# Kernel optimization log

Hardware: AMD Instinct MI355X
Metric: run time of the kernel (lower is better)

Reference implementation:

```python
import jax, jax.numpy as jnp
import numpy as np

M = 28            # mask head resolution (mask_logit[i] is MxM)
NUM_CLASSES = 80  # max value of cls_idx (mask_image channel count)


def setup_inputs() -> dict:
    key = jax.random.key(0)
    k1, k2, k3, k4, k5, k6, k7 = jax.random.split(key, 7)
    N, H, W = 100, 800, 800
    cx = jax.random.uniform(k1, (N,), minval=0.0, maxval=float(W - 1))
    cy = jax.random.uniform(k2, (N,), minval=0.0, maxval=float(H - 1))
    bw = jax.random.uniform(k3, (N,), minval=20.0, maxval=300.0)
    bh = jax.random.uniform(k4, (N,), minval=20.0, maxval=300.0)
    mask_rois = jnp.stack([cx - bw / 2, cy - bh / 2, cx + bw / 2, cy + bh / 2], axis=1).astype(jnp.float32)
    cls_prob = jax.random.uniform(k5, (N,), dtype=jnp.float32)
    mask_prob = jax.random.normal(k6, (N, M, M), dtype=jnp.float32)
    cls_idx = jax.random.randint(k7, (N,), 1, NUM_CLASSES + 1, dtype=jnp.int32)
    return {"mask_rois": mask_rois, "cls_prob": cls_prob, "mask_prob": mask_prob,
            "cls_idx": cls_idx, "im_h": H, "im_w": W}


def _paste(logit, box, H, W):
    """Bilinear-paste an MxM logit into the full HxW image (== cv2.resize to (w,h)
    then placing at the box, evaluated directly on image pixel coords)."""
    x0, y0, x1, y1 = box[0], box[1], box[2], box[3]  # int32
    w = jnp.maximum(x1 - x0 + 1, 1).astype(jnp.float32)
    h = jnp.maximum(y1 - y0 + 1, 1).astype(jnp.float32)
    xs = jnp.arange(W, dtype=jnp.float32)
    ys = jnp.arange(H, dtype=jnp.float32)
    # cv2 bilinear mapping: src = (dst + 0.5) * (M / size) - 0.5, clamped at borders
    sx = jnp.clip((xs - x0.astype(jnp.float32) + 0.5) * (M / w) - 0.5, 0.0, M - 1.0)
    sy = jnp.clip((ys - y0.astype(jnp.float32) + 0.5) * (M / h) - 0.5, 0.0, M - 1.0)
    ix0 = jnp.floor(sx).astype(jnp.int32); ix1 = jnp.minimum(ix0 + 1, M - 1); fx = sx - ix0
    iy0 = jnp.floor(sy).astype(jnp.int32); iy1 = jnp.minimum(iy0 + 1, M - 1); fy = sy - iy0
    v00 = logit[iy0[:, None], ix0[None, :]]
    v01 = logit[iy0[:, None], ix1[None, :]]
    v10 = logit[iy1[:, None], ix0[None, :]]
    v11 = logit[iy1[:, None], ix1[None, :]]
    val = ((1 - fy)[:, None] * ((1 - fx)[None, :] * v00 + fx[None, :] * v01)
           + fy[:, None] * ((1 - fx)[None, :] * v10 + fx[None, :] * v11))
    xi = jnp.arange(W, dtype=jnp.int32)
    yi = jnp.arange(H, dtype=jnp.int32)
    inside_x = (xi >= jnp.maximum(x0, 0)) & (xi < jnp.minimum(x1 + 1, W))
    inside_y = (yi >= jnp.maximum(y0, 0)) & (yi < jnp.minimum(y1 + 1, H))
    inside = inside_y[:, None] & inside_x[None, :]
    return jnp.where(inside, val, 0.0), inside


def _forward(mask_rois, cls_prob, mask_prob, cls_idx, H, W, thr):
    N = mask_prob.shape[0]
    order = jnp.argsort(-cls_prob)                       # sort by score, descending
    boxes = mask_rois[order].astype(jnp.int32)
    logits = mask_prob[order]
    cls = cls_idx[order].astype(jnp.int32) - 1           # 0-based class ids
    pasted, inside = jax.vmap(lambda l, b: _paste(l, b, H, W))(logits, boxes)  # [N,H,W]

    def step(mask_image, xs):
        logit, ins, c = xs
        mask = (logit > 0) & ins                          # thresholded, in-image crop mask
        prev = mask_image[c]
        msum = jnp.sum(mask).astype(jnp.float32)
        ovl = jnp.sum(mask & prev).astype(jnp.float32)    # overlap with accumulated class mask
        keep = (msum > 0) & (ovl <= thr * msum)           # skip if ratio > threshold
        mask_image = mask_image.at[c].set(prev | (mask & keep))
        return mask_image, keep

    mask_image0 = jnp.zeros((NUM_CLASSES, H, W), dtype=bool)
    _, keep = jax.lax.scan(step, mask_image0, (pasted, inside, cls))

    # compact kept masks to the front (frame_id order); dropped boxes go to slot N (discarded)
    pos = jnp.where(keep, jnp.cumsum(keep.astype(jnp.int32)) - 1, N)
    energy = jnp.where(inside & keep[:, None, None], pasted, 0.0)
    full = jnp.zeros((N + 1, H, W), pasted.dtype).at[pos].set(energy)
    mask_energy = full[:N][None]                          # [1, N, H, W], kept masks first
    keep_inds = jnp.full((N + 1,), -1, jnp.int32).at[pos].set(
        jnp.where(keep, order.astype(jnp.int32), -1))[:N]
    return keep_inds, mask_energy


def reference(mask_rois, cls_prob, mask_prob, cls_idx, im_h, im_w):
    return _forward(mask_rois, cls_prob, mask_prob, cls_idx, int(im_h), int(im_w), 0.3)
```

## Files before the change

kernel.cpp:

```cpp
#include <hip/hip_runtime.h>

#define NINST 100
#define MLOG 28
#define IMG 800
#define LOGSZ (MLOG * MLOG)

#define OFF_ORDER 0
#define OFF_CLS   100
#define OFF_BOX   200
#define OFF_MSUM  600
#define OFF_SLOT  800
#define OFF_NK    900
#define OFF_OVL   1024
#define OFF_MASK  11264
#define ROWW      12
#define MSTRIDE   (ROWW * 304)
#define F4TOT     (NINST * IMG * IMG / 4)
#define NZB       4096

__device__ __forceinline__ bool box_ovl(const int* sb, int a, int b2) {
    int axs = max(sb[4 * a], 0), axe = min(sb[4 * a + 2] + 1, IMG);
    int ays = max(sb[4 * a + 1], 0), aye = min(sb[4 * a + 3] + 1, IMG);
    int bxs = max(sb[4 * b2], 0), bxe = min(sb[4 * b2 + 2] + 1, IMG);
    int bys = max(sb[4 * b2 + 1], 0), bye = min(sb[4 * b2 + 3] + 1, IMG);
    return axs < bxe && bxs < axe && ays < bye && bys < aye;
}

__global__ __launch_bounds__(256) void k_mask(const float* __restrict__ mask_prob,
                                              const float* __restrict__ cls_prob,
                                              const float* __restrict__ rois,
                                              const int* __restrict__ cls_idx,
                                              int* __restrict__ ws) {
    int b = blockIdx.x, tid = threadIdx.x;
    __shared__ float s_p[NINST];
    __shared__ int s_order[NINST];
    __shared__ float lg[LOGSZ];
    __shared__ int red[256];
    if (tid < NINST) s_p[tid] = cls_prob[tid];
    __syncthreads();
    if (tid < NINST) {
        float p = s_p[tid];
        int r = 0;
        for (int j = 0; j < NINST; j++) {
            float q = s_p[j];
            r += (q > p) || (q == p && j < tid);
        }
        s_order[r] = tid;
    }
    __syncthreads();
    int n = b;
    int orig = s_order[n];
    int x0 = (int)rois[4 * orig], y0 = (int)rois[4 * orig + 1];
    int x1 = (int)rois[4 * orig + 2], y1 = (int)rois[4 * orig + 3];
    if (b == 0 && tid < NINST) {
        int o = s_order[tid];
        ws[OFF_ORDER + tid] = o;
        ws[OFF_CLS + tid] = cls_idx[o] - 1;
#pragma unroll
        for (int k = 0; k < 4; k++)
            ws[OFF_BOX + 4 * tid + k] = (int)rois[4 * o + k];
    }
    for (int i = tid; i < LOGSZ; i += 256) lg[i] = mask_prob[orig * LOGSZ + i];
    __syncthreads();
    int xs = max(x0, 0), xe = min(x1 + 1, IMG);
    int ys = max(y0, 0), ye = min(y1 + 1, IMG);
    int wx0 = xs >> 5, nw = ((xe + 31) >> 5) - wx0, nrows = ye - ys;
    float wf = fmaxf((float)(x1 - x0 + 1), 1.f), hf = fmaxf((float)(y1 - y0 + 1), 1.f);
    float rx = 28.f / wf, ry = 28.f / hf;
    unsigned* mb = (unsigned*)(ws + OFF_MASK) + n * MSTRIDE;
    int total = nrows * nw, cnt = 0;
    for (int t = tid; t < total; t += 256) {
        int row = t / nw, wc = t - row * nw;
        int y = ys + row;
        float sy = ((float)y - (float)y0 + 0.5f) * ry - 0.5f;
        sy = fminf(fmaxf(sy, 0.f), 27.f);
        int iy0 = (int)sy, iy1 = min(iy0 + 1, 27);
        float fy = sy - (float)iy0;
        const float* r0 = lg + iy0 * MLOG;
        const float* r1 = lg + iy1 * MLOG;
        unsigned bits = 0u;
        int xbase = (wx0 + wc) << 5;
        int j0 = max(xs - xbase, 0), j1 = min(xe - xbase, 32);
        for (int j = j0; j < j1; j++) {
            int xx = xbase + j;
            float sx = ((float)xx - (float)x0 + 0.5f) * rx - 0.5f;
            sx = fminf(fmaxf(sx, 0.f), 27.f);
            int ix0 = (int)sx, ix1 = min(ix0 + 1, 27);
            float fx = sx - (float)ix0;
            float val = (1.f - fy) * ((1.f - fx) * r0[ix0] + fx * r0[ix1]) +
                        fy * ((1.f - fx) * r1[ix0] + fx * r1[ix1]);
            bits |= (val > 0.f) ? (1u << j) : 0u;
        }
        mb[row * ROWW + wc] = bits;
        cnt += __popc(bits);
    }
    red[tid] = cnt;
    __syncthreads();
    for (int s = 128; s; s >>= 1) {
        if (tid < s) red[tid] += red[tid + s];
        __syncthreads();
    }
    if (tid == 0) ws[OFF_MSUM + n] = red[0];
}

__global__ __launch_bounds__(64) void k_pairs(int* __restrict__ ws) {
    int i = blockIdx.x, j = blockIdx.y, tid = threadIdx.x;
    if (i >= j) return;
    if (ws[OFF_CLS + i] != ws[OFF_CLS + j]) return;
    if (ws[OFF_MSUM + i] == 0 || ws[OFF_MSUM + j] == 0) return;
    const int* bi = ws + OFF_BOX + 4 * i;
    const int* bj = ws + OFF_BOX + 4 * j;
    int ixs = max(bi[0], 0), ixe = min(bi[2] + 1, IMG);
    int iys = max(bi[1], 0), iye = min(bi[3] + 1, IMG);
    int jxs = max(bj[0], 0), jxe = min(bj[2] + 1, IMG);
    int jys = max(bj[1], 0), jye = min(bj[3] + 1, IMG);
    if (!(ixs < jxe && jxs < ixe && iys < jye && jys < iye)) return;
    int iwx0 = ixs >> 5, jwx0 = jxs >> 5;
    int wlo = max(iwx0, jwx0);
    int whi = min((ixe + 31) >> 5, (jxe + 31) >> 5);
    int rlo = max(iys, jys), rhi = min(iye, jye);
    int nw = whi - wlo, nrows = rhi - rlo;
    const unsigned* mi = (const unsigned*)(ws + OFF_MASK) + i * MSTRIDE;
    const unsigned* mj = (const unsigned*)(ws + OFF_MASK) + j * MSTRIDE;
    int total = nrows * nw, cnt = 0;
    for (int t = tid; t < total; t += 64) {
        int row = t / nw, wc = t - row * nw;
        int y = rlo + row, w = wlo + wc;
        cnt += __popc(mi[(y - iys) * ROWW + (w - iwx0)] &
                      mj[(y - jys) * ROWW + (w - jwx0)]);
    }
    for (int off = 32; off; off >>= 1) cnt += __shfl_down(cnt, off);
    if (tid == 0) ws[OFF_OVL + i * NINST + j] = cnt;
}

__global__ __launch_bounds__(256) void k_scan_zero(int* __restrict__ ws, float* __restrict__ out) {
    int b = blockIdx.x, tid = threadIdx.x;
    if (b > 0) {
        float4* outv = (float4*)(out + NINST);
        for (size_t pi = (size_t)(b - 1) * 256 + tid; pi < F4TOT; pi += (size_t)NZB * 256)
            outv[pi] = make_float4(0.f, 0.f, 0.f, 0.f);
        return;
    }
    __shared__ int s_ovl[NINST * NINST];
    __shared__ int s_cls[NINST], s_msum[NINST], s_box[4 * NINST];
    for (int i = tid; i < NINST * NINST; i += 256) s_ovl[i] = ws[OFF_OVL + i];
    for (int i = tid; i < NINST; i += 256) {
        s_cls[i] = ws[OFF_CLS + i];
        s_msum[i] = ws[OFF_MSUM + i];
    }
    for (int i = tid; i < 4 * NINST; i += 256) s_box[i] = ws[OFF_BOX + i];
    __syncthreads();
    if (tid >= 64) return;
    int ln = tid;
    const unsigned* maskbase = (const unsigned*)(ws + OFF_MASK);

    unsigned long long k0 = 0ull, k1 = 0ull;
    for (int n = 0; n < NINST; n++) {
        int msum = s_msum[n];
        if (msum == 0) continue;
        int pb = 64 + ln;
        bool ca = (ln < n) && s_cls[ln] == s_cls[n] && ((k0 >> ln) & 1ull) && box_ovl(s_box, ln, n);
        bool cb = (pb < n) && s_cls[pb] == s_cls[n] && ((k1 >> ln) & 1ull) && box_ovl(s_box, pb, n);
        int oa = ca ? s_ovl[ln * NINST + n] : 0;
        int ob = cb ? s_ovl[pb * NINST + n] : 0;
        int sum = oa + ob, mx = max(oa, ob);
        for (int off = 32; off; off >>= 1) {
            sum += __shfl_down(sum, off);
            mx = max(mx, __shfl_down(mx, off));
        }
        int keep = 0, need = 0;
        if (ln == 0) {
            float t = 0.3f * (float)msum;
            if ((float)sum <= t) keep = 1;
            else if ((float)mx > t) keep = 0;
            else need = 1;
        }
        keep = __shfl(keep, 0);
        need = __shfl(need, 0);
        if (need) {
            unsigned long long ba = __ballot(ca), bb = __ballot(cb);
            int nxs = max(s_box[4 * n], 0), nxe = min(s_box[4 * n + 2] + 1, IMG);
            int nys = max(s_box[4 * n + 1], 0), nye = min(s_box[4 * n + 3] + 1, IMG);
            int wx0 = nxs >> 5, nw = ((nxe + 31) >> 5) - wx0, nrows = nye - nys;
            const unsigned* mn = maskbase + n * MSTRIDE;
            int total = nrows * nw, ovl = 0;
            for (int t2 = ln; t2 < total; t2 += 64) {
                int row = t2 / nw, wc = t2 - row * nw;
                unsigned bits = mn[row * ROWW + wc];
                if (!bits) continue;
                int y = nys + row, wa = wx0 + wc;
                unsigned img = 0;
                unsigned long long rem = ba;
                while (rem) {
                    int m = __ffsll((long long)rem) - 1; rem &= rem - 1;
                    int mys = max(s_box[4 * m + 1], 0), mye = min(s_box[4 * m + 3] + 1, IMG);
                    int mxs = max(s_box[4 * m], 0), mxe = min(s_box[4 * m + 2] + 1, IMG);
                    int mwx0 = mxs >> 5, mnw = ((mxe + 31) >> 5) - mwx0;
                    int rr = y - mys, cc = wa - mwx0;
                    if (rr >= 0 && rr < (mye - mys) && cc >= 0 && cc < mnw)
                        img |= maskbase[m * MSTRIDE + rr * ROWW + cc];
                }
                rem = bb;
                while (rem) {
                    int m0 = __ffsll((long long)rem) - 1; rem &= rem - 1;
                    int m = 64 + m0;
                    int mys = max(s_box[4 * m + 1], 0), mye = min(s_box[4 * m + 3] + 1, IMG);
                    int mxs = max(s_box[4 * m], 0), mxe = min(s_box[4 * m + 2] + 1, IMG);
                    int mwx0 = mxs >> 5, mnw = ((mxe + 31) >> 5) - mwx0;
                    int rr = y - mys, cc = wa - mwx0;
                    if (rr >= 0 && rr < (mye - mys) && cc >= 0 && cc < mnw)
                        img |= maskbase[m * MSTRIDE + rr * ROWW + cc];
                }
                ovl += __popc(bits & img);
            }
            for (int off = 32; off; off >>= 1) ovl += __shfl_down(ovl, off);
            if (ln == 0) keep = ((float)ovl <= 0.3f * (float)msum);
            keep = __shfl(keep, 0);
        }
        if (keep) {
            if (n < 64) k0 |= 1ull << n;
            else k1 |= 1ull << (n - 64);
        }
    }

    int nk = __popcll(k0) + __popcll(k1);
    if (ln == 0) ws[OFF_NK] = nk;
    unsigned long long lm = (ln == 0) ? 0ull : (~0ull >> (64 - ln));
    if ((k0 >> ln) & 1ull) {
        int pos = __popcll(k0 & lm);
        ws[OFF_SLOT + pos] = ln;
        out[pos] = (float)ws[OFF_ORDER + ln];
    }
    if (ln < 36 && ((k1 >> ln) & 1ull)) {
        int pos = __popcll(k0) + __popcll(k1 & lm);
        ws[OFF_SLOT + pos] = 64 + ln;
        out[pos] = (float)ws[OFF_ORDER + 64 + ln];
    }
    for (int s = ln; s < NINST; s += 64)
        if (s >= nk) out[s] = -1.f;
}

__global__ __launch_bounds__(256) void k_box(const float* __restrict__ mask_prob,
                                             const int* __restrict__ ws,
                                             float* __restrict__ out) {
    int slot = blockIdx.y, tid = threadIdx.x;
    if (slot >= ws[OFF_NK]) return;
    int n = ws[OFF_SLOT + slot];
    const int* box = ws + OFF_BOX + 4 * n;
    int x0 = box[0], y0 = box[1], x1 = box[2], y1 = box[3];
    int xs = max(x0, 0), xe = min(x1 + 1, IMG);
    int ys = max(y0, 0), ye = min(y1 + 1, IMG);
    int xa = xs & ~3;
    int w4 = (xe - xa + 3) >> 2;
    int rows = ye - ys;
    int total4 = rows * w4;
    __shared__ float lg[LOGSZ];
    int orig = ws[OFF_ORDER + n];
    for (int i = tid; i < LOGSZ; i += 256) lg[i] = mask_prob[orig * LOGSZ + i];
    __syncthreads();
    float wf = fmaxf((float)(x1 - x0 + 1), 1.f), hf = fmaxf((float)(y1 - y0 + 1), 1.f);
    float rx = 28.f / wf, ry = 28.f / hf;
    float* base = out + NINST + (size_t)slot * (IMG * IMG);
    for (int t = blockIdx.x * 256 + tid; t < total4; t += gridDim.x * 256) {
        int row = t / w4, c4 = t - row * w4;
        int y = ys + row, xb = xa + (c4 << 2);
        float sy = ((float)y - (float)y0 + 0.5f) * ry - 0.5f;
        sy = fminf(fmaxf(sy, 0.f), 27.f);
        int iy0 = (int)sy, iy1 = min(iy0 + 1, 27);
        float fy = sy - (float)iy0;
        const float* r0 = lg + iy0 * MLOG;
        const float* r1 = lg + iy1 * MLOG;
        float v[4];
#pragma unroll
        for (int j = 0; j < 4; j++) {
            int xx = xb + j;
            float val = 0.f;
            if (xx >= xs && xx < xe) {
                float sx = ((float)xx - (float)x0 + 0.5f) * rx - 0.5f;
                sx = fminf(fmaxf(sx, 0.f), 27.f);
                int ix0 = (int)sx, ix1 = min(ix0 + 1, 27);
                float fx = sx - (float)ix0;
                val = (1.f - fy) * ((1.f - fx) * r0[ix0] + fx * r0[ix1]) +
                      fy * ((1.f - fx) * r1[ix0] + fx * r1[ix1]);
            }
            v[j] = val;
        }
        *(float4*)(base + (size_t)y * IMG + xb) = make_float4(v[0], v[1], v[2], v[3]);
    }
}

extern "C" void kernel_launch(void* const* d_in, const int* in_sizes, int n_in,
                              void* d_out, int out_size, void* d_ws, size_t ws_size,
                              hipStream_t stream) {
    const float* rois      = (const float*)d_in[0];
    const float* cls_prob  = (const float*)d_in[1];
    const float* mask_prob = (const float*)d_in[2];
    const int*   cls_idx   = (const int*)d_in[3];
    int* ws = (int*)d_ws;
    float* out = (float*)d_out;

    k_mask<<<dim3(NINST), dim3(256), 0, stream>>>(mask_prob, cls_prob, rois, cls_idx, ws);
    k_pairs<<<dim3(NINST, NINST), dim3(64), 0, stream>>>(ws);
    k_scan_zero<<<dim3(NZB + 1), dim3(256), 0, stream>>>(ws, out);
    k_box<<<dim3(91, NINST), dim3(256), 0, stream>>>(mask_prob, ws, out);
}
```

Baseline: 357.1 us.

## Fuse pair-overlap, keep scan and paste into one persistent kernel with grid barriers

Replaces the pairs, scan-plus-zero and box kernels with a single persistent kernel of 512 blocks that uses software grid barriers. Pair overlaps are compacted into a small atomic list rather than a dense 100x100 matrix. Each output plane is written exactly once, as either zeros or pasted values, which removes the separate full-image zeroing pass and its double write. The risks are spin-barrier deadlock if all 512 blocks are not co-resident, and a fallback to the slow path when the pair list overflows its 256 capacity.

After: 470.2 us. 31.7% more time.

```diff
diff --git a/kernel.cpp b/kernel.cpp
--- a/kernel.cpp
+++ b/kernel.cpp
@@ -4,6 +4,10 @@
 #define MLOG 28
 #define IMG 800
 #define LOGSZ (MLOG * MLOG)
+#define NBLK2 512
+#define PCAP  256
+#define PL4   (IMG * IMG / 4)
+#define CH4   (PL4 / 5)
 
 #define OFF_ORDER 0
 #define OFF_CLS   100
@@ -11,12 +15,14 @@
 #define OFF_MSUM  600
 #define OFF_SLOT  800
 #define OFF_NK    900
-#define OFF_OVL   1024
+#define OFF_NPAIR 901
+#define OFF_BAR   904
+#define OFF_PAIRS 1024
 #define OFF_MASK  11264
 #define ROWW      12
 #define MSTRIDE   (ROWW * 304)
-#define F4TOT     (NINST * IMG * IMG / 4)
-#define NZB       4096
+
+#define AGENT __HIP_MEMORY_SCOPE_AGENT
 
 __device__ __forceinline__ bool box_ovl(const int* sb, int a, int b2) {
     int axs = max(sb[4 * a], 0), axe = min(sb[4 * a + 2] + 1, IMG);
@@ -24,6 +30,17 @@
     int bxs = max(sb[4 * b2], 0), bxe = min(sb[4 * b2 + 2] + 1, IMG);
     int bys = max(sb[4 * b2 + 1], 0), bye = min(sb[4 * b2 + 3] + 1, IMG);
     return axs < bxe && bxs < axe && ays < bye && bys < aye;
+}
+
+__device__ __forceinline__ void gbar(int* cnt, int nblk) {
+    __syncthreads();
+    if (threadIdx.x == 0) {
+        __threadfence();
+        __hip_atomic_fetch_add(cnt, 1, __ATOMIC_RELEASE, AGENT);
+        while (__hip_atomic_load(cnt, __ATOMIC_ACQUIRE, AGENT) < nblk)
+            __builtin_amdgcn_s_sleep(8);
+    }
+    __syncthreads();
 }
 
 __global__ __launch_bounds__(256) void k_mask(const float* __restrict__ mask_prob,
@@ -52,13 +69,20 @@
     int orig = s_order[n];
     int x0 = (int)rois[4 * orig], y0 = (int)rois[4 * orig + 1];
     int x1 = (int)rois[4 * orig + 2], y1 = (int)rois[4 * orig + 3];
-    if (b == 0 && tid < NINST) {
-        int o = s_order[tid];
-        ws[OFF_ORDER + tid] = o;
-        ws[OFF_CLS + tid] = cls_idx[o] - 1;
+    if (b == 0) {
+        if (tid == 0) {
+            ws[OFF_NPAIR] = 0;
+            ws[OFF_BAR] = 0;
+            ws[OFF_BAR + 1] = 0;
+        }
+        if (tid < NINST) {
+            int o = s_order[tid];
+            ws[OFF_ORDER + tid] = o;
+            ws[OFF_CLS + tid] = cls_idx[o] - 1;
 #pragma unroll
-        for (int k = 0; k < 4; k++)
-            ws[OFF_BOX + 4 * tid + k] = (int)rois[4 * o + k];
+            for (int k = 0; k < 4; k++)
+                ws[OFF_BOX + 4 * tid + k] = (int)rois[4 * o + k];
+        }
     }
     for (int i = tid; i < LOGSZ; i += 256) lg[i] = mask_prob[orig * LOGSZ + i];
     __syncthreads();
@@ -103,189 +127,216 @@
     if (tid == 0) ws[OFF_MSUM + n] = red[0];
 }
 
-__global__ __launch_bounds__(64) void k_pairs(int* __restrict__ ws) {
-    int i = blockIdx.x, j = blockIdx.y, tid = threadIdx.x;
-    if (i >= j) return;
-    if (ws[OFF_CLS + i] != ws[OFF_CLS + j]) return;
-    if (ws[OFF_MSUM + i] == 0 || ws[OFF_MSUM + j] == 0) return;
-    const int* bi = ws + OFF_BOX + 4 * i;
-    const int* bj = ws + OFF_BOX + 4 * j;
-    int ixs = max(bi[0], 0), ixe = min(bi[2] + 1, IMG);
-    int iys = max(bi[1], 0), iye = min(bi[3] + 1, IMG);
-    int jxs = max(bj[0], 0), jxe = min(bj[2] + 1, IMG);
-    int jys = max(bj[1], 0), jye = min(bj[3] + 1, IMG);
-    if (!(ixs < jxe && jxs < ixe && iys < jye && jys < iye)) return;
-    int iwx0 = ixs >> 5, jwx0 = jxs >> 5;
-    int wlo = max(iwx0, jwx0);
-    int whi = min((ixe + 31) >> 5, (jxe + 31) >> 5);
-    int rlo = max(iys, jys), rhi = min(iye, jye);
-    int nw = whi - wlo, nrows = rhi - rlo;
-    const unsigned* mi = (const unsigned*)(ws + OFF_MASK) + i * MSTRIDE;
-    const unsigned* mj = (const unsigned*)(ws + OFF_MASK) + j * MSTRIDE;
-    int total = nrows * nw, cnt = 0;
-    for (int t = tid; t < total; t += 64) {
-        int row = t / nw, wc = t - row * nw;
-        int y = rlo + row, w = wlo + wc;
-        cnt += __popc(mi[(y - iys) * ROWW + (w - iwx0)] &
-                      mj[(y - jys) * ROWW + (w - jwx0)]);
-    }
-    for (int off = 32; off; off >>= 1) cnt += __shfl_down(cnt, off);
-    if (tid == 0) ws[OFF_OVL + i * NINST + j] = cnt;
-}
-
-__global__ __launch_bounds__(256) void k_scan_zero(int* __restrict__ ws, float* __restrict__ out) {
+__global__ __launch_bounds__(256, 2) void k_fused(const float* __restrict__ mask_prob,
+                                                  int* __restrict__ ws,
+                                                  float* __restrict__ out) {
     int b = blockIdx.x, tid = threadIdx.x;
-    if (b > 0) {
-        float4* outv = (float4*)(out + NINST);
-        for (size_t pi = (size_t)(b - 1) * 256 + tid; pi < F4TOT; pi += (size_t)NZB * 256)
-            outv[pi] = make_float4(0.f, 0.f, 0.f, 0.f);
-        return;
-    }
     __shared__ int s_ovl[NINST * NINST];
     __shared__ int s_cls[NINST], s_msum[NINST], s_box[4 * NINST];
-    for (int i = tid; i < NINST * NINST; i += 256) s_ovl[i] = ws[OFF_OVL + i];
-    for (int i = tid; i < NINST; i += 256) {
-        s_cls[i] = ws[OFF_CLS + i];
-        s_msum[i] = ws[OFF_MSUM + i];
-    }
-    for (int i = tid; i < 4 * NINST; i += 256) s_box[i] = ws[OFF_BOX + i];
-    __syncthreads();
-    if (tid >= 64) return;
-    int ln = tid;
+    __shared__ float lg[LOGSZ];
     const unsigned* maskbase = (const unsigned*)(ws + OFF_MASK);
 
-    unsigned long long k0 = 0ull, k1 = 0ull;
-    for (int n = 0; n < NINST; n++) {
-        int msum = s_msum[n];
-        if (msum == 0) continue;
-        int pb = 64 + ln;
-        bool ca = (ln < n) && s_cls[ln] == s_cls[n] && ((k0 >> ln) & 1ull) && box_ovl(s_box, ln, n);
-        bool cb = (pb < n) && s_cls[pb] == s_cls[n] && ((k1 >> ln) & 1ull) && box_ovl(s_box, pb, n);
-        int oa = ca ? s_ovl[ln * NINST + n] : 0;
-        int ob = cb ? s_ovl[pb * NINST + n] : 0;
-        int sum = oa + ob, mx = max(oa, ob);
-        for (int off = 32; off; off >>= 1) {
-            sum += __shfl_down(sum, off);
-            mx = max(mx, __shfl_down(mx, off));
-        }
-        int keep = 0, need = 0;
-        if (ln == 0) {
-            float t = 0.3f * (float)msum;
-            if ((float)sum <= t) keep = 1;
-            else if ((float)mx > t) keep = 0;
-            else need = 1;
-        }
-        keep = __shfl(keep, 0);
-        need = __shfl(need, 0);
-        if (need) {
-            unsigned long long ba = __ballot(ca), bb = __ballot(cb);
-            int nxs = max(s_box[4 * n], 0), nxe = min(s_box[4 * n + 2] + 1, IMG);
-            int nys = max(s_box[4 * n + 1], 0), nye = min(s_box[4 * n + 3] + 1, IMG);
-            int wx0 = nxs >> 5, nw = ((nxe + 31) >> 5) - wx0, nrows = nye - nys;
-            const unsigned* mn = maskbase + n * MSTRIDE;
-            int total = nrows * nw, ovl = 0;
-            for (int t2 = ln; t2 < total; t2 += 64) {
-                int row = t2 / nw, wc = t2 - row * nw;
-                unsigned bits = mn[row * ROWW + wc];
-                if (!bits) continue;
-                int y = nys + row, wa = wx0 + wc;
-                unsigned img = 0;
-                unsigned long long rem = ba;
-                while (rem) {
-                    int m = __ffsll((long long)rem) - 1; rem &= rem - 1;
-                    int mys = max(s_box[4 * m + 1], 0), mye = min(s_box[4 * m + 3] + 1, IMG);
-                    int mxs = max(s_box[4 * m], 0), mxe = min(s_box[4 * m + 2] + 1, IMG);
-                    int mwx0 = mxs >> 5, mnw = ((mxe + 31) >> 5) - mwx0;
-                    int rr = y - mys, cc = wa - mwx0;
-                    if (rr >= 0 && rr < (mye - mys) && cc >= 0 && cc < mnw)
-                        img |= maskbase[m * MSTRIDE + rr * ROWW + cc];
-                }
-                rem = bb;
-                while (rem) {
-                    int m0 = __ffsll((long long)rem) - 1; rem &= rem - 1;
-                    int m = 64 + m0;
-                    int mys = max(s_box[4 * m + 1], 0), mye = min(s_box[4 * m + 3] + 1, IMG);
-                    int mxs = max(s_box[4 * m], 0), mxe = min(s_box[4 * m + 2] + 1, IMG);
-                    int mwx0 = mxs >> 5, mnw = ((mxe + 31) >> 5) - mwx0;
-                    int rr = y - mys, cc = wa - mwx0;
-                    if (rr >= 0 && rr < (mye - mys) && cc >= 0 && cc < mnw)
-                        img |= maskbase[m * MSTRIDE + rr * ROWW + cc];
-                }
-                ovl += __popc(bits & img);
-            }
-            for (int off = 32; off; off >>= 1) ovl += __shfl_down(ovl, off);
-            if (ln == 0) keep = ((float)ovl <= 0.3f * (float)msum);
-            keep = __shfl(keep, 0);
-        }
-        if (keep) {
-            if (n < 64) k0 |= 1ull << n;
-            else k1 |= 1ull << (n - 64);
-        }
-    }
-
-    int nk = __popcll(k0) + __popcll(k1);
-    if (ln == 0) ws[OFF_NK] = nk;
-    unsigned long long lm = (ln == 0) ? 0ull : (~0ull >> (64 - ln));
-    if ((k0 >> ln) & 1ull) {
-        int pos = __popcll(k0 & lm);
-        ws[OFF_SLOT + pos] = ln;
-        out[pos] = (float)ws[OFF_ORDER + ln];
-    }
-    if (ln < 36 && ((k1 >> ln) & 1ull)) {
-        int pos = __popcll(k0) + __popcll(k1 & lm);
-        ws[OFF_SLOT + pos] = 64 + ln;
-        out[pos] = (float)ws[OFF_ORDER + 64 + ln];
-    }
-    for (int s = ln; s < NINST; s += 64)
-        if (s >= nk) out[s] = -1.f;
-}
-
-__global__ __launch_bounds__(256) void k_box(const float* __restrict__ mask_prob,
-                                             const int* __restrict__ ws,
-                                             float* __restrict__ out) {
-    int slot = blockIdx.y, tid = threadIdx.x;
-    if (slot >= ws[OFF_NK]) return;
-    int n = ws[OFF_SLOT + slot];
+    {
+        int wid = b * 4 + (tid >> 6), ln = tid & 63;
+        for (int p = wid; p < NINST * NINST; p += NBLK2 * 4) {
+            int i = p / NINST, j = p - i * NINST;
+            if (i >= j) continue;
+            if (ws[OFF_CLS + i] != ws[OFF_CLS + j]) continue;
+            if (ws[OFF_MSUM + i] == 0 || ws[OFF_MSUM + j] == 0) continue;
+            const int* bi = ws + OFF_BOX + 4 * i;
+            const int* bj = ws + OFF_BOX + 4 * j;
+            int ixs = max(bi[0], 0), ixe = min(bi[2] + 1, IMG);
+            int iys = max(bi[1], 0), iye = min(bi[3] + 1, IMG);
+            int jxs = max(bj[0], 0), jxe = min(bj[2] + 1, IMG);
+            int jys = max(bj[1], 0), jye = min(bj[3] + 1, IMG);
+            if (!(ixs < jxe && jxs < ixe && iys < jye && jys < iye)) continue;
+            int iwx0 = ixs >> 5, jwx0 = jxs >> 5;
+            int wlo = max(iwx0, jwx0);
+            int whi = min((ixe + 31) >> 5, (jxe + 31) >> 5);
+            int rlo = max(iys, jys), rhi = min(iye, jye);
+            int nw = whi - wlo, nrows = rhi - rlo;
+            const unsigned* mi = maskbase + i * MSTRIDE;
+            const unsigned* mj = maskbase + j * MSTRIDE;
+            int total = nrows * nw, cnt = 0;
+            for (int t = ln; t < total; t += 64) {
+                int row = t / nw, wc = t - row * nw;
+                int y = rlo + row, w = wlo + wc;
+                cnt += __popc(mi[(y - iys) * ROWW + (w - iwx0)] &
+                              mj[(y - jys) * ROWW + (w - jwx0)]);
+            }
+            for (int off = 32; off; off >>= 1) cnt += __shfl_down(cnt, off);
+            if (ln == 0) {
+                int k = __hip_atomic_fetch_add(ws + OFF_NPAIR, 1, __ATOMIC_RELAXED, AGENT);
+                if (k < PCAP) {
+                    __hip_atomic_store(ws + OFF_PAIRS + 3 * k, i, __ATOMIC_RELAXED, AGENT);
+                    __hip_atomic_store(ws + OFF_PAIRS + 3 * k + 1, j, __ATOMIC_RELAXED, AGENT);
+                    __hip_atomic_store(ws + OFF_PAIRS + 3 * k + 2, cnt, __ATOMIC_RELAXED, AGENT);
+                }
+            }
+        }
+    }
+    gbar(ws + OFF_BAR, NBLK2);
+
+    if (b == 0) {
+        for (int q = tid; q < NINST * NINST; q += 256) s_ovl[q] = 0;
+        for (int q = tid; q < NINST; q += 256) {
+            s_cls[q] = ws[OFF_CLS + q];
+            s_msum[q] = ws[OFF_MSUM + q];
+        }
+        for (int q = tid; q < 4 * NINST; q += 256) s_box[q] = ws[OFF_BOX + q];
+        int npr = __hip_atomic_load(ws + OFF_NPAIR, __ATOMIC_RELAXED, AGENT);
+        int np = min(npr, PCAP);
+        bool pov = (npr > PCAP);
+        __syncthreads();
+        for (int q = tid; q < np; q += 256) {
+            int i = __hip_atomic_load(ws + OFF_PAIRS + 3 * q, __ATOMIC_RELAXED, AGENT);
+            int j = __hip_atomic_load(ws + OFF_PAIRS + 3 * q + 1, __ATOMIC_RELAXED, AGENT);
+            int c = __hip_atomic_load(ws + OFF_PAIRS + 3 * q + 2, __ATOMIC_RELAXED, AGENT);
+            s_ovl[i * NINST + j] = c;
+        }
+        __syncthreads();
+        if (tid < 64) {
+            int ln = tid;
+            unsigned long long k0 = 0ull, k1 = 0ull;
+            for (int n = 0; n < NINST; n++) {
+                int msum = s_msum[n];
+                if (msum == 0) continue;
+                int pb = 64 + ln;
+                bool ca = (ln < n) && s_cls[ln] == s_cls[n] && ((k0 >> ln) & 1ull) && box_ovl(s_box, ln, n);
+                bool cb = (pb < n) && s_cls[pb] == s_cls[n] && ((k1 >> ln) & 1ull) && box_ovl(s_box, pb, n);
+                int oa = ca ? s_ovl[ln * NINST + n] : 0;
+                int ob = cb ? s_ovl[pb * NINST + n] : 0;
+                int sum = oa + ob, mx = max(oa, ob);
+                for (int off = 32; off; off >>= 1) {
+                    sum += __shfl_down(sum, off);
+                    mx = max(mx, __shfl_down(mx, off));
+                }
+                unsigned long long anyc = __ballot(ca || cb);
+                int keep = 0, need = 0;
+                if (ln == 0) {
+                    float t = 0.3f * (float)msum;
+                    if (pov) { need = (anyc != 0ull); keep = (!need); }
+                    else if ((float)sum <= t) keep = 1;
+                    else if ((float)mx > t) keep = 0;
+                    else need = 1;
+                }
+                keep = __shfl(keep, 0);
+                need = __shfl(need, 0);
+                if (need) {
+                    unsigned long long ba = __ballot(ca), bb = __ballot(cb);
+                    int nxs = max(s_box[4 * n], 0), nxe = min(s_box[4 * n + 2] + 1, IMG);
+                    int nys = max(s_box[4 * n + 1], 0), nye = min(s_box[4 * n + 3] + 1, IMG);
+                    int wx0 = nxs >> 5, nw = ((nxe + 31) >> 5) - wx0, nrows = nye - nys;
+                    const unsigned* mn = maskbase + n * MSTRIDE;
+                    int total = nrows * nw, ovl = 0;
+                    for (int t2 = ln; t2 < total; t2 += 64) {
+                        int row = t2 / nw, wc = t2 - row * nw;
+                        unsigned bits = mn[row * ROWW + wc];
+                        if (!bits) continue;
+                        int y = nys + row, wa = wx0 + wc;
+                        unsigned img = 0;
+                        unsigned long long rem = ba;
+                        while (rem) {
+                            int m = __ffsll((long long)rem) - 1; rem &= rem - 1;
+                            int mys = max(s_box[4 * m + 1], 0), mye = min(s_box[4 * m + 3] + 1, IMG);
+                            int mxs = max(s_box[4 * m], 0), mxe = min(s_box[4 * m + 2] + 1, IMG);
+                            int mwx0 = mxs >> 5, mnw = ((mxe + 31) >> 5) - mwx0;
+                            int rr = y - mys, cc = wa - mwx0;
+                            if (rr >= 0 && rr < (mye - mys) && cc >= 0 && cc < mnw)
+                                img |= maskbase[m * MSTRIDE + rr * ROWW + cc];
+                        }
+                        rem = bb;
+                        while (rem) {
+                            int m0 = __ffsll((long long)rem) - 1; rem &= rem - 1;
+                            int m = 64 + m0;
+                            int mys = max(s_box[4 * m + 1], 0), mye = min(s_box[4 * m + 3] + 1, IMG);
+                            int mxs = max(s_box[4 * m], 0), mxe = min(s_box[4 * m + 2] + 1, IMG);
+                            int mwx0 = mxs >> 5, mnw = ((mxe + 31) >> 5) - mwx0;
+                            int rr = y - mys, cc = wa - mwx0;
+                            if (rr >= 0 && rr < (mye - mys) && cc >= 0 && cc < mnw)
+                                img |= maskbase[m * MSTRIDE + rr * ROWW + cc];
+                        }
+                        ovl += __popc(bits & img);
+                    }
+                    for (int off = 32; off; off >>= 1) ovl += __shfl_down(ovl, off);
+                    if (ln == 0) keep = ((float)ovl <= 0.3f * (float)msum);
+                    keep = __shfl(keep, 0);
+                }
+                if (keep) {
+                    if (n < 64) k0 |= 1ull << n;
+                    else k1 |= 1ull << (n - 64);
+                }
+            }
+            int nk = __popcll(k0) + __popcll(k1);
+            if (ln == 0) __hip_atomic_store(ws + OFF_NK, nk, __ATOMIC_RELAXED, AGENT);
+            unsigned long long lm = (ln == 0) ? 0ull : (~0ull >> (64 - ln));
+            if ((k0 >> ln) & 1ull) {
+                int pos = __popcll(k0 & lm);
+                __hip_atomic_store(ws + OFF_SLOT + pos, ln, __ATOMIC_RELAXED, AGENT);
+                out[pos] = (float)ws[OFF_ORDER + ln];
+            }
+            if (ln < 36 && ((k1 >> ln) & 1ull)) {
+                int pos = __popcll(k0) + __popcll(k1 & lm);
+                __hip_atomic_store(ws + OFF_SLOT + pos, 64 + ln, __ATOMIC_RELAXED, AGENT);
+                out[pos] = (float)ws[OFF_ORDER + 64 + ln];
+            }
+            for (int s = ln; s < NINST; s += 64)
+                if (s >= nk) out[s] = -1.f;
+        }
+        __syncthreads();
+    }
+    gbar(ws + OFF_BAR + 1, NBLK2);
+
+    if (b >= 5 * NINST) return;
+    int slot = b / 5, chunk = b - 5 * slot;
+    int nk = __hip_atomic_load(ws + OFF_NK, __ATOMIC_RELAXED, AGENT);
+    float4* plane = (float4*)(out + NINST) + (size_t)slot * PL4;
+    int base4 = chunk * CH4;
+    if (slot >= nk) {
+        float4 z = make_float4(0.f, 0.f, 0.f, 0.f);
+        for (int i = tid; i < CH4; i += 256) plane[base4 + i] = z;
+        return;
+    }
+    int n = __hip_atomic_load(ws + OFF_SLOT + slot, __ATOMIC_RELAXED, AGENT);
+    int orig = ws[OFF_ORDER + n];
     const int* box = ws + OFF_BOX + 4 * n;
     int x0 = box[0], y0 = box[1], x1 = box[2], y1 = box[3];
     int xs = max(x0, 0), xe = min(x1 + 1, IMG);
     int ys = max(y0, 0), ye = min(y1 + 1, IMG);
-    int xa = xs & ~3;
-    int w4 = (xe - xa + 3) >> 2;
-    int rows = ye - ys;
-    int total4 = rows * w4;
-    __shared__ float lg[LOGSZ];
-    int orig = ws[OFF_ORDER + n];
     for (int i = tid; i < LOGSZ; i += 256) lg[i] = mask_prob[orig * LOGSZ + i];
     __syncthreads();
     float wf = fmaxf((float)(x1 - x0 + 1), 1.f), hf = fmaxf((float)(y1 - y0 + 1), 1.f);
     float rx = 28.f / wf, ry = 28.f / hf;
-    float* base = out + NINST + (size_t)slot * (IMG * IMG);
-    for (int t = blockIdx.x * 256 + tid; t < total4; t += gridDim.x * 256) {
-        int row = t / w4, c4 = t - row * w4;
-        int y = ys + row, xb = xa + (c4 << 2);
-        float sy = ((float)y - (float)y0 + 0.5f) * ry - 0.5f;
-        sy = fminf(fmaxf(sy, 0.f), 27.f);
-        int iy0 = (int)sy, iy1 = min(iy0 + 1, 27);
-        float fy = sy - (float)iy0;
-        const float* r0 = lg + iy0 * MLOG;
-        const float* r1 = lg + iy1 * MLOG;
-        float v[4];
+    for (int i = tid; i < CH4; i += 256) {
+        int idx4 = base4 + i;
+        int y = idx4 / (IMG / 4);
+        int xb = (idx4 - y * (IMG / 4)) * 4;
+        float4 res = make_float4(0.f, 0.f, 0.f, 0.f);
+        if (y >= ys && y < ye && xb + 3 >= xs && xb < xe) {
+            float sy = ((float)y - (float)y0 + 0.5f) * ry - 0.5f;
+            sy = fminf(fmaxf(sy, 0.f), 27.f);
+            int iy0 = (int)sy, iy1 = min(iy0 + 1, 27);
+            float fy = sy - (float)iy0;
+            const float* r0 = lg + iy0 * MLOG;
+            const float* r1 = lg + iy1 * MLOG;
+            float v[4];
 #pragma unroll
-        for (int j = 0; j < 4; j++) {
-            int xx = xb + j;
-            float val = 0.f;
-            if (xx >= xs && xx < xe) {
-                float sx = ((float)xx - (float)x0 + 0.5f) * rx - 0.5f;
-                sx = fminf(fmaxf(sx, 0.f), 27.f);
-                int ix0 = (int)sx, ix1 = min(ix0 + 1, 27);
-                float fx = sx - (float)ix0;
-                val = (1.f - fy) * ((1.f - fx) * r0[ix0] + fx * r0[ix1]) +
-                      fy * ((1.f - fx) * r1[ix0] + fx * r1[ix1]);
-            }
-            v[j] = val;
-        }
-        *(float4*)(base + (size_t)y * IMG + xb) = make_float4(v[0], v[1], v[2], v[3]);
+            for (int j = 0; j < 4; j++) {
+                int xx = xb + j;
+                float val = 0.f;
+                if (xx >= xs && xx < xe) {
+                    float sx = ((float)xx - (float)x0 + 0.5f) * rx - 0.5f;
+                    sx = fminf(fmaxf(sx, 0.f), 27.f);
+                    int ix0 = (int)sx, ix1 = min(ix0 + 1, 27);
+                    float fx = sx - (float)ix0;
+                    val = (1.f - fy) * ((1.f - fx) * r0[ix0] + fx * r0[ix1]) +
+                          fy * ((1.f - fx) * r1[ix0] + fx * r1[ix1]);
+                }
+                v[j] = val;
+            }
+            res = make_float4(v[0], v[1], v[2], v[3]);
+        }
+        plane[idx4] = res;
     }
 }
 
@@ -300,7 +351,5 @@
     float* out = (float*)d_out;
 
     k_mask<<<dim3(NINST), dim3(256), 0, stream>>>(mask_prob, cls_prob, rois, cls_idx, ws);
-    k_pairs<<<dim3(NINST, NINST), dim3(64), 0, stream>>>(ws);
-    k_scan_zero<<<dim3(NZB + 1), dim3(256), 0, stream>>>(ws, out);
-    k_box<<<dim3(91, NINST), dim3(256), 0, stream>>>(mask_prob, ws, out);
-}
+    k_fused<<<dim3(NBLK2), dim3(256), 0, stream>>>(mask_prob, ws, out);
+}
```
